# Kernel tuning notes

Hardware: AMD Instinct MI355X
Metric: run time of the kernel (lower is better)

Reference implementation:

```python
import jax, jax.numpy as jnp
import numpy as np

B, T, N, E = 8, 12, 10000, 160000
TD, OD = 64, 64  # temporal_dim, output_dim
EPS = 1e-5


def _ln(x, g, b):
    m = jnp.mean(x, axis=-1, keepdims=True)
    v = jnp.var(x, axis=-1, keepdims=True)
    return (x - m) * jax.lax.rsqrt(v + EPS) * g + b


def _gcn_agg(feat, src, dst, n_nodes):
    # feat: [B, N, D]; mean aggregation of src features into dst nodes
    msgs = feat[:, src, :]                                   # [B, E, D]
    deg = jnp.zeros((n_nodes,), feat.dtype).at[dst].add(1.0)  # [N]
    agg = jnp.zeros_like(feat).at[:, dst, :].add(msgs)        # [B, N, D]
    return agg / jnp.maximum(deg, 1.0)[None, :, None]


def setup_inputs() -> dict:
    key = jax.random.key(0)
    ks = jax.random.split(key, 20)
    s = 0.05
    rn = lambda k, shape: jax.random.normal(k, shape, jnp.float32) * s
    return {
        "x": jax.random.normal(ks[0], (B, T, N), jnp.float32),
        "edge_index": jax.random.randint(ks[1], (2, E), 0, N),
        "causal_edge_index": jax.random.randint(ks[2], (2, E), 0, N),
        # temporal branches (Linear over T)
        "W_ht": rn(ks[3], (T, TD)), "b_ht": jnp.zeros((TD,), jnp.float32),
        "W_lt": rn(ks[4], (T, TD)), "b_lt": jnp.zeros((TD,), jnp.float32),
        # high-freq spatial GCN
        "Ws_h": rn(ks[5], (TD, OD)), "Wn_h": rn(ks[6], (TD, OD)), "b_h": jnp.zeros((OD,), jnp.float32),
        # low-freq spatial GCN (base + causal graph)
        "Ws_l": rn(ks[7], (TD, OD)), "Wn_l": rn(ks[8], (TD, OD)), "Wc_l": rn(ks[9], (TD, OD)), "b_l": jnp.zeros((OD,), jnp.float32),
        # residual projections
        "Whr": rn(ks[10], (TD, OD)), "bhr": jnp.zeros((OD,), jnp.float32),
        "Wlr": rn(ks[11], (TD, OD)), "blr": jnp.zeros((OD,), jnp.float32),
        # layer norms
        "g_hn": jnp.ones((OD,), jnp.float32), "b_hn": jnp.zeros((OD,), jnp.float32),
        "g_ln": jnp.ones((OD,), jnp.float32), "b_ln": jnp.zeros((OD,), jnp.float32),
        # attention fusion gate
        "Wa": rn(ks[12], (2 * OD, 2)), "ba": jnp.zeros((2,), jnp.float32),
        # global residual
        "Wg": rn(ks[13], (T, OD)), "bg": jnp.zeros((OD,), jnp.float32),
        "g_gn": jnp.ones((OD,), jnp.float32), "b_gn": jnp.zeros((OD,), jnp.float32),
    }


def reference(x, edge_index, causal_edge_index,
              W_ht, b_ht, W_lt, b_lt,
              Ws_h, Wn_h, b_h, Ws_l, Wn_l, Wc_l, b_l,
              Whr, bhr, Wlr, blr,
              g_hn, b_hn, g_ln, b_ln,
              Wa, ba, Wg, bg, g_gn, b_gn):
    Bx, Tx, Nx = x.shape
    src, dst = edge_index[0], edge_index[1]
    csrc, cdst = causal_edge_index[0], causal_edge_index[1]
    x_for_residual = x + x  # low_src + high_src (both = x in source)

    # --- high-frequency branch ---
    ht = jnp.einsum('btn,td->bnd', x, W_ht) + b_ht          # [B, N, TD]
    agg_h = _gcn_agg(ht, src, dst, Nx)
    high = ht @ Ws_h + agg_h @ Wn_h + b_h                   # [B, N, OD]
    high = high + 0.2 * (ht @ Whr + bhr)
    high = _ln(high, g_hn, b_hn)
    high = jnp.where(high >= 0, high, 0.1 * high)           # leaky_relu(0.1)

    # --- low-frequency branch ---
    lt = jnp.einsum('btn,td->bnd', x, W_lt) + b_lt          # [B, N, TD]
    agg_l = _gcn_agg(lt, src, dst, Nx)
    agg_c = _gcn_agg(lt, csrc, cdst, Nx)
    low = lt @ Ws_l + agg_l @ Wn_l + agg_c @ Wc_l + b_l     # [B, N, OD]
    low = low + 0.2 * (lt @ Wlr + blr)
    low = _ln(low, g_ln, b_ln)
    low = jax.nn.gelu(low, approximate=False)

    # --- attention fusion ---
    logits = jnp.concatenate([high, low], axis=-1) @ Wa + ba  # [B, N, 2]
    a = jax.nn.softmax(logits, axis=-1)
    fused = a[..., 0:1] * high + a[..., 1:2] * low
    fused = fused + 0.3 * high + 0.3 * low

    # --- global residual ---
    residual = jnp.einsum('btn,td->bnd', x_for_residual, Wg) + bg
    residual = _ln(residual, g_gn, b_gn)
    fused = fused + 0.1 * residual

    # return in original [B, output_dim, N] layout
    return (jnp.swapaxes(fused, 1, 2), jnp.swapaxes(high, 1, 2), jnp.swapaxes(low, 1, 2))
```

## Files before the change

### kernel.cpp

```cpp
#include <hip/hip_runtime.h>

#define B_ 8
#define T_ 12
#define N_ 10000
#define E_ 160000
#define NQ_ 24
#define EPS_ 1e-5f
#define CAP_ 64
#define NC32 313
#define NT64 157

#define O_PAR     0
#define O_CURA    24576
#define O_CURC    65536
#define O_SLOTA   106496
#define O_SLOTC   2666496
#define O_XT      5226496

#define P_TAIL 4608

template<int CTRL>
__device__ __forceinline__ float dpp_add(float v) {
    int s = __builtin_amdgcn_update_dpp(0, __float_as_int(v), CTRL, 0xF, 0xF, true);
    return v + __int_as_float(s);
}
__device__ __forceinline__ float wave_sum(float v) {
    v = dpp_add<0x111>(v);
    v = dpp_add<0x112>(v);
    v = dpp_add<0x114>(v);
    v = dpp_add<0x118>(v);
    v = dpp_add<0x142>(v);
    v = dpp_add<0x143>(v);
    return __int_as_float(__builtin_amdgcn_readlane(__float_as_int(v), 63));
}

__device__ __forceinline__ void prep_task(int task,
    const float* W_ht, const float* W_lt,
    const float* Ws_h, const float* Wn_h,
    const float* Ws_l, const float* Wn_l, const float* Wc_l,
    const float* Whr, const float* Wlr,
    const float* Wg, float* par)
{
    int t = task >> 6, d = task & 63;
    float ah = 0.f, bh = 0.f, al = 0.f, bl = 0.f, cl = 0.f;
    for (int k = 0; k < 64; ++k) {
        float msh = Ws_h[k * 64 + d] + 0.2f * Whr[k * 64 + d];
        float msl = Ws_l[k * 64 + d] + 0.2f * Wlr[k * 64 + d];
        float wht = W_ht[t * 64 + k];
        float wlt = W_lt[t * 64 + k];
        ah += wht * msh;
        bh += wht * Wn_h[k * 64 + d];
        al += wlt * msl;
        bl += wlt * Wn_l[k * 64 + d];
        cl += wlt * Wc_l[k * 64 + d];
    }
    par[d * 72 + 0 * 12 + t] = ah;
    par[d * 72 + 1 * 12 + t] = bh;
    par[d * 72 + 2 * 12 + t] = al;
    par[d * 72 + 3 * 12 + t] = bl;
    par[d * 72 + 4 * 12 + t] = cl;
    par[d * 72 + 5 * 12 + t] = 2.f * Wg[t * 64 + d];
}

__device__ __forceinline__ void prep_tail(int d,
    const float* b_ht, const float* b_lt,
    const float* Ws_h, const float* Wn_h, const float* b_h,
    const float* Ws_l, const float* Wn_l, const float* Wc_l, const float* b_l,
    const float* Whr, const float* bhr, const float* Wlr, const float* blr,
    float* par)
{
    float ch0 = b_h[d] + 0.2f * bhr[d];
    float ch1 = 0.f;
    float cl0 = b_l[d] + 0.2f * blr[d];
    float cl1 = 0.f, cl2 = 0.f;
    for (int k = 0; k < 64; ++k) {
        float bht = b_ht[k];
        float blt = b_lt[k];
        float msh = Ws_h[k * 64 + d] + 0.2f * Whr[k * 64 + d];
        float msl = Ws_l[k * 64 + d] + 0.2f * Wlr[k * 64 + d];
        ch0 += bht * msh;
        ch1 += bht * Wn_h[k * 64 + d];
        cl0 += blt * msl;
        cl1 += blt * Wn_l[k * 64 + d];
        cl2 += blt * Wc_l[k * 64 + d];
    }
    par[P_TAIL + 0 * 64 + d] = ch0;
    par[P_TAIL + 1 * 64 + d] = ch1;
    par[P_TAIL + 2 * 64 + d] = cl0;
    par[P_TAIL + 3 * 64 + d] = cl1;
    par[P_TAIL + 4 * 64 + d] = cl2;
}

__global__ __launch_bounds__(256) void k1_kernel(
    const float* __restrict__ x, float* __restrict__ xt,
    const int* __restrict__ ei, const int* __restrict__ cei,
    int* __restrict__ curA, int* __restrict__ curC,
    int* __restrict__ slotA, int* __restrict__ slotC,
    const float* W_ht, const float* b_ht, const float* W_lt, const float* b_lt,
    const float* Ws_h, const float* Wn_h, const float* b_h,
    const float* Ws_l, const float* Wn_l, const float* Wc_l, const float* b_l,
    const float* Whr, const float* bhr, const float* Wlr, const float* blr,
    const float* Wg, float* par)
{
    __shared__ float tld[64 * 98];
    const int tid = threadIdx.x;
    const int blk = blockIdx.x;

    if (blk < NT64) {
        const int n0 = blk * 64;
        const int j = tid & 63;
        const int r0 = tid >> 6;
        const bool ok = (n0 + j) < N_;
#pragma unroll
        for (int rr = 0; rr < 24; ++rr) {
            int r = rr * 4 + r0;
            tld[j * 98 + r] = ok ? x[r * N_ + n0 + j] : 0.f;
        }
        __syncthreads();
        float4* xt4 = (float4*)xt;
#pragma unroll
        for (int it = 0; it < 6; ++it) {
            int idx = it * 256 + tid;
            int jj = idx / 24, q = idx - jj * 24;
            if (n0 + jj < N_) {
                float4 v;
                v.x = tld[jj * 98 + 4 * q + 0];
                v.y = tld[jj * 98 + 4 * q + 1];
                v.z = tld[jj * 98 + 4 * q + 2];
                v.w = tld[jj * 98 + 4 * q + 3];
                xt4[(size_t)(n0 + jj) * NQ_ + q] = v;
            }
        }
        return;
    }
    if (blk < NT64 + 3) {
        int task = (blk - NT64) * 256 + tid;
        prep_task(task, W_ht, W_lt, Ws_h, Wn_h, Ws_l, Wn_l, Wc_l, Whr, Wlr, Wg, par);
        return;
    }
    if (blk == NT64 + 3) {
        if (tid < 64)
            prep_tail(tid, b_ht, b_lt, Ws_h, Wn_h, b_h, Ws_l, Wn_l, Wc_l, b_l,
                      Whr, bhr, Wlr, blr, par);
        return;
    }
    int i = (blk - NT64 - 4) * 256 + tid;
    if (i < E_) {
        int dd = ei[E_ + i];
        int p = atomicAdd(&curA[dd], 1);
        if (p < CAP_) slotA[dd * CAP_ + p] = ei[i];
    } else if (i < 2 * E_) {
        int e = i - E_;
        int dd = cei[E_ + e];
        int p = atomicAdd(&curC[dd], 1);
        if (p < CAP_) slotC[dd * CAP_ + p] = cei[e];
    }
}

__global__ __launch_bounds__(256, 4) void main_kernel(
    const float* __restrict__ x, const float* __restrict__ par,
    const float4* __restrict__ xt4,
    const int* __restrict__ curA, const int* __restrict__ curC,
    const int* __restrict__ slotA, const int* __restrict__ slotC,
    const float* __restrict__ g_hn, const float* __restrict__ b_hn,
    const float* __restrict__ g_ln, const float* __restrict__ b_ln,
    const float* __restrict__ Wa, const float* __restrict__ ba,
    const float* __restrict__ bg, const float* __restrict__ g_gn,
    const float* __restrict__ b_gn,
    float* __restrict__ out)
{
    __shared__ __align__(16) float s_out[3][64 * 33];
    __shared__ __align__(16) float xs[32 * 12];
    __shared__ __align__(16) float as_[32 * 12];
    __shared__ __align__(16) float cs_[32 * 12];
    __shared__ float indA[32];
    __shared__ float indC[32];

    const int tid = threadIdx.x;
    const int lane = tid & 63;
    const int wave = tid >> 6;
    const int b = blockIdx.x & 7;
    const int n0 = (blockIdx.x >> 3) * 32;
    const int d = lane;

    {
        int idx = tid;
        int t = idx >> 5, node = idx & 31;
        int n = n0 + node;
        xs[node * 12 + t] = (n < N_) ? x[(b * T_ + t) * N_ + n] : 0.f;
        idx = tid + 256;
        if (idx < 384) {
            t = idx >> 5; node = idx & 31; n = n0 + node;
            xs[node * 12 + t] = (n < N_) ? x[(b * T_ + t) * N_ + n] : 0.f;
        }
    }

    {
        float4* P4 = (float4*)&s_out[0][0];
        const int p = tid >> 2;
        const int s = tid & 3;
        const int node = p & 31;
        const int set = p >> 5;
        const int n = n0 + node;
        float4 a0 = {0,0,0,0}, a1 = {0,0,0,0}, a2 = {0,0,0,0};
        if (n < N_) {
            const int* sl = (set ? slotC : slotA) + n * CAP_;
            int dgRaw = (set ? curC : curA)[n];
            int dg = dgRaw < CAP_ ? dgRaw : CAP_;
            for (int j = s; j < dg; j += 4) {
                const float4* src = xt4 + (size_t)sl[j] * NQ_ + b * 3;
                float4 v0 = src[0], v1 = src[1], v2 = src[2];
                a0.x += v0.x; a0.y += v0.y; a0.z += v0.z; a0.w += v0.w;
                a1.x += v1.x; a1.y += v1.y; a1.z += v1.z; a1.w += v1.w;
                a2.x += v2.x; a2.y += v2.y; a2.z += v2.z; a2.w += v2.w;
            }
        }
        P4[tid * 3 + 0] = a0;
        P4[tid * 3 + 1] = a1;
        P4[tid * 3 + 2] = a2;
    }
    __syncthreads();
    {
        const float4* P4 = (const float4*)&s_out[0][0];
        if (tid < 192) {
            int p2 = tid / 3, q = tid - p2 * 3;
            int node = p2 & 31, set = p2 >> 5;
            int n = n0 + node;
            float4 s0 = P4[(p2 * 4 + 0) * 3 + q];
            float4 s1 = P4[(p2 * 4 + 1) * 3 + q];
            float4 s2 = P4[(p2 * 4 + 2) * 3 + q];
            float4 s3 = P4[(p2 * 4 + 3) * 3 + q];
            float4 sum;
            sum.x = (s0.x + s1.x) + (s2.x + s3.x);
            sum.y = (s0.y + s1.y) + (s2.y + s3.y);
            sum.z = (s0.z + s1.z) + (s2.z + s3.z);
            sum.w = (s0.w + s1.w) + (s2.w + s3.w);
            int dgRaw = (n < N_) ? (set ? curC : curA)[n] : 0;
            float inv = 1.f / (float)(dgRaw > 0 ? dgRaw : 1);
            sum.x *= inv; sum.y *= inv; sum.z *= inv; sum.w *= inv;
            ((float4*)(set ? cs_ : as_))[node * 3 + q] = sum;
        } else {
            int i = tid - 192;
            int node = i & 31, set = i >> 5;
            int n = n0 + node;
            float f = (n < N_ && (set ? curC : curA)[n] > 0) ? 1.f : 0.f;
            if (set) indC[node] = f; else indA[node] = f;
        }
    }

    float w[72];
    {
        const float4* wv = (const float4*)(par + d * 72);
#pragma unroll
        for (int k = 0; k < 18; ++k) ((float4*)w)[k] = wv[k];
    }
    const float ch0 = par[P_TAIL + 0 * 64 + d], ch1 = par[P_TAIL + 1 * 64 + d];
    const float cl0 = par[P_TAIL + 2 * 64 + d], cl1 = par[P_TAIL + 3 * 64 + d];
    const float cl2 = par[P_TAIL + 4 * 64 + d];
    const float ghn = g_hn[d], bhn = b_hn[d];
    const float gln = g_ln[d], bln = b_ln[d];
    const float ggn = g_gn[d], bgn = b_gn[d];
    const float bgd = bg[d];
    const float wd0 = Wa[d * 2 + 0] - Wa[d * 2 + 1];
    const float wd1 = Wa[(64 + d) * 2 + 0] - Wa[(64 + d) * 2 + 1];
    const float bad = ba[0] - ba[1];

    __syncthreads();

#pragma unroll 2
    for (int i = 0; i < 8; ++i) {
        const int nl = wave * 8 + i;
        float u[12], ua[12], uc[12];
#pragma unroll
        for (int k = 0; k < 3; ++k) {
            ((float4*)u)[k]  = ((const float4*)(xs  + nl * 12))[k];
            ((float4*)ua)[k] = ((const float4*)(as_ + nl * 12))[k];
            ((float4*)uc)[k] = ((const float4*)(cs_ + nl * 12))[k];
        }
        const float indd = indA[nl], indc = indC[nl];

        float acc_h = ch0 + indd * ch1;
        float acc_l = cl0 + indd * cl1 + indc * cl2;
        float acc_r = bgd;
#pragma unroll
        for (int t = 0; t < 12; ++t) {
            acc_h += u[t] * w[t]      + ua[t] * w[12 + t];
            acc_l += u[t] * w[24 + t] + ua[t] * w[36 + t] + uc[t] * w[48 + t];
            acc_r += u[t] * w[60 + t];
        }

        float v0 = wave_sum(acc_h);
        float v1 = wave_sum(acc_h * acc_h);
        float v2 = wave_sum(acc_l);
        float v3 = wave_sum(acc_l * acc_l);
        float v4 = wave_sum(acc_r);
        float v5 = wave_sum(acc_r * acc_r);

        const float mh = v0 * (1.f / 64.f);
        const float varh = fmaxf(v1 * (1.f / 64.f) - mh * mh, 0.f);
        float hn = (acc_h - mh) * rsqrtf(varh + EPS_) * ghn + bhn;
        float high = hn >= 0.f ? hn : 0.1f * hn;

        const float ml = v2 * (1.f / 64.f);
        const float varl = fmaxf(v3 * (1.f / 64.f) - ml * ml, 0.f);
        float lnv = (acc_l - ml) * rsqrtf(varl + EPS_) * gln + bln;
        float low = 0.5f * lnv * (1.f + erff(lnv * 0.70710678118654752f));

        const float mr = v4 * (1.f / 64.f);
        const float varr = fmaxf(v5 * (1.f / 64.f) - mr * mr, 0.f);
        float rn = (acc_r - mr) * rsqrtf(varr + EPS_) * ggn + bgn;

        float S = wave_sum(high * wd0 + low * wd1);
        float a0 = 1.f / (1.f + expf(-(S + bad)));
        float fused = a0 * high + (1.f - a0) * low + 0.3f * high + 0.3f * low + 0.1f * rn;

        s_out[0][d * 33 + nl] = fused;
        s_out[1][d * 33 + nl] = high;
        s_out[2][d * 33 + nl] = low;
    }
    __syncthreads();

    const int off1 = B_ * 64 * N_;
    const int off2 = 2 * B_ * 64 * N_;
    for (int e2 = tid; e2 < 64 * 32; e2 += 256) {
        int r = e2 >> 5, nl = e2 & 31;
        int n = n0 + nl;
        if (n < N_) {
            float* o = out + (b * 64 + r) * N_ + n;
            o[0]    = s_out[0][r * 33 + nl];
            o[off1] = s_out[1][r * 33 + nl];
            o[off2] = s_out[2][r * 33 + nl];
        }
    }
}

extern "C" void kernel_launch(void* const* d_in, const int* in_sizes, int n_in,
                              void* d_out, int out_size, void* d_ws, size_t ws_size,
                              hipStream_t stream)
{
    const float* x   = (const float*)d_in[0];
    const int* ei    = (const int*)d_in[1];
    const int* cei   = (const int*)d_in[2];
    const float* W_ht = (const float*)d_in[3];
    const float* b_ht = (const float*)d_in[4];
    const float* W_lt = (const float*)d_in[5];
    const float* b_lt = (const float*)d_in[6];
    const float* Ws_h = (const float*)d_in[7];
    const float* Wn_h = (const float*)d_in[8];
    const float* b_h  = (const float*)d_in[9];
    const float* Ws_l = (const float*)d_in[10];
    const float* Wn_l = (const float*)d_in[11];
    const float* Wc_l = (const float*)d_in[12];
    const float* b_l  = (const float*)d_in[13];
    const float* Whr  = (const float*)d_in[14];
    const float* bhr  = (const float*)d_in[15];
    const float* Wlr  = (const float*)d_in[16];
    const float* blr  = (const float*)d_in[17];
    const float* g_hn = (const float*)d_in[18];
    const float* b_hn = (const float*)d_in[19];
    const float* g_ln = (const float*)d_in[20];
    const float* b_ln = (const float*)d_in[21];
    const float* Wa   = (const float*)d_in[22];
    const float* ba   = (const float*)d_in[23];
    const float* Wg   = (const float*)d_in[24];
    const float* bg   = (const float*)d_in[25];
    const float* g_gn = (const float*)d_in[26];
    const float* b_gn = (const float*)d_in[27];

    char* ws = (char*)d_ws;
    float* par   = (float*)(ws + O_PAR);
    int* curA    = (int*)(ws + O_CURA);
    int* curC    = (int*)(ws + O_CURC);
    int* slotA   = (int*)(ws + O_SLOTA);
    int* slotC   = (int*)(ws + O_SLOTC);
    float* xt    = (float*)(ws + O_XT);

    hipMemsetAsync(ws + O_CURA, 0, O_SLOTA - O_CURA, stream);

    k1_kernel<<<NT64 + 4 + (2 * E_ + 255) / 256, 256, 0, stream>>>(
        x, xt, ei, cei, curA, curC, slotA, slotC,
        W_ht, b_ht, W_lt, b_lt, Ws_h, Wn_h, b_h,
        Ws_l, Wn_l, Wc_l, b_l, Whr, bhr, Wlr, blr, Wg, par);

    main_kernel<<<NC32 * 8, 256, 0, stream>>>(
        x, par, (const float4*)xt, curA, curC, slotA, slotC,
        g_hn, b_hn, g_ln, b_ln, Wa, ba, bg, g_gn, b_gn, (float*)d_out);
}
```

Measured before the change: 208.5 us.

## Vectorize edge binning, unroll neighbor gather by two, use fast reciprocal/exp

Each thread in the edge-binning phase now loads four edges at once with int4 loads and issues four atomics, so the grid shrinks to match. The neighbor gather loop is unrolled to process two neighbors per iteration, which puts more loads in flight. The degree reciprocal and the attention sigmoid now use hardware rcp and fast exp intrinsics, and the high/low stores are moved ahead of the wave reduction. The fast intrinsics can slightly change numerics, and the int4 loads assume the edge arrays are 16-byte aligned.

```diff
diff --git a/kernel.cpp b/kernel.cpp
--- a/kernel.cpp
+++ b/kernel.cpp
@@ -144,16 +144,30 @@
                       Whr, bhr, Wlr, blr, par);
         return;
     }
-    int i = (blk - NT64 - 4) * 256 + tid;
-    if (i < E_) {
-        int dd = ei[E_ + i];
-        int p = atomicAdd(&curA[dd], 1);
-        if (p < CAP_) slotA[dd * CAP_ + p] = ei[i];
-    } else if (i < 2 * E_) {
-        int e = i - E_;
-        int dd = cei[E_ + e];
-        int p = atomicAdd(&curC[dd], 1);
-        if (p < CAP_) slotC[dd * CAP_ + p] = cei[e];
+    int e4 = (blk - NT64 - 4) * 256 + tid;
+    if (e4 < E_ / 4) {
+        int4 s4 = *(const int4*)&ei[4 * e4];
+        int4 d4 = *(const int4*)&ei[E_ + 4 * e4];
+        int p0 = atomicAdd(&curA[d4.x], 1);
+        int p1 = atomicAdd(&curA[d4.y], 1);
+        int p2 = atomicAdd(&curA[d4.z], 1);
+        int p3 = atomicAdd(&curA[d4.w], 1);
+        if (p0 < CAP_) slotA[d4.x * CAP_ + p0] = s4.x;
+        if (p1 < CAP_) slotA[d4.y * CAP_ + p1] = s4.y;
+        if (p2 < CAP_) slotA[d4.z * CAP_ + p2] = s4.z;
+        if (p3 < CAP_) slotA[d4.w * CAP_ + p3] = s4.w;
+    } else if (e4 < 2 * (E_ / 4)) {
+        int q = e4 - E_ / 4;
+        int4 s4 = *(const int4*)&cei[4 * q];
+        int4 d4 = *(const int4*)&cei[E_ + 4 * q];
+        int p0 = atomicAdd(&curC[d4.x], 1);
+        int p1 = atomicAdd(&curC[d4.y], 1);
+        int p2 = atomicAdd(&curC[d4.z], 1);
+        int p3 = atomicAdd(&curC[d4.w], 1);
+        if (p0 < CAP_) slotC[d4.x * CAP_ + p0] = s4.x;
+        if (p1 < CAP_) slotC[d4.y * CAP_ + p1] = s4.y;
+        if (p2 < CAP_) slotC[d4.z * CAP_ + p2] = s4.z;
+        if (p3 < CAP_) slotC[d4.w * CAP_ + p3] = s4.w;
     }
 }
 
@@ -207,7 +221,17 @@
             const int* sl = (set ? slotC : slotA) + n * CAP_;
             int dgRaw = (set ? curC : curA)[n];
             int dg = dgRaw < CAP_ ? dgRaw : CAP_;
-            for (int j = s; j < dg; j += 4) {
+            int j = s;
+            for (; j + 4 < dg; j += 8) {
+                const float4* src0 = xt4 + (size_t)sl[j]     * NQ_ + b * 3;
+                const float4* src1 = xt4 + (size_t)sl[j + 4] * NQ_ + b * 3;
+                float4 v0 = src0[0], v1 = src0[1], v2 = src0[2];
+                float4 v3 = src1[0], v4 = src1[1], v5 = src1[2];
+                a0.x += v0.x + v3.x; a0.y += v0.y + v3.y; a0.z += v0.z + v3.z; a0.w += v0.w + v3.w;
+                a1.x += v1.x + v4.x; a1.y += v1.y + v4.y; a1.z += v1.z + v4.z; a1.w += v1.w + v4.w;
+                a2.x += v2.x + v5.x; a2.y += v2.y + v5.y; a2.z += v2.z + v5.z; a2.w += v2.w + v5.w;
+            }
+            if (j < dg) {
                 const float4* src = xt4 + (size_t)sl[j] * NQ_ + b * 3;
                 float4 v0 = src[0], v1 = src[1], v2 = src[2];
                 a0.x += v0.x; a0.y += v0.y; a0.z += v0.z; a0.w += v0.w;
@@ -236,7 +260,7 @@
             sum.z = (s0.z + s1.z) + (s2.z + s3.z);
             sum.w = (s0.w + s1.w) + (s2.w + s3.w);
             int dgRaw = (n < N_) ? (set ? curC : curA)[n] : 0;
-            float inv = 1.f / (float)(dgRaw > 0 ? dgRaw : 1);
+            float inv = __builtin_amdgcn_rcpf((float)(dgRaw > 0 ? dgRaw : 1));
             sum.x *= inv; sum.y *= inv; sum.z *= inv; sum.w *= inv;
             ((float4*)(set ? cs_ : as_))[node * 3 + q] = sum;
         } else {
@@ -310,13 +334,14 @@
         const float varr = fmaxf(v5 * (1.f / 64.f) - mr * mr, 0.f);
         float rn = (acc_r - mr) * rsqrtf(varr + EPS_) * ggn + bgn;
 
-        float S = wave_sum(high * wd0 + low * wd1);
-        float a0 = 1.f / (1.f + expf(-(S + bad)));
-        float fused = a0 * high + (1.f - a0) * low + 0.3f * high + 0.3f * low + 0.1f * rn;
-
-        s_out[0][d * 33 + nl] = fused;
         s_out[1][d * 33 + nl] = high;
         s_out[2][d * 33 + nl] = low;
+
+        float S = wave_sum(high * wd0 + low * wd1);
+        float a0 = __builtin_amdgcn_rcpf(1.f + __expf(-(S + bad)));
+        float fused = a0 * high + (1.f - a0) * low + 0.3f * high + 0.3f * low + 0.1f * rn;
+
+        s_out[0][d * 33 + nl] = fused;
     }
     __syncthreads();
 
@@ -377,7 +402,7 @@
 
     hipMemsetAsync(ws + O_CURA, 0, O_SLOTA - O_CURA, stream);
 
-    k1_kernel<<<NT64 + 4 + (2 * E_ + 255) / 256, 256, 0, stream>>>(
+    k1_kernel<<<NT64 + 4 + 313, 256, 0, stream>>>(
         x, xt, ei, cei, curA, curC, slotA, slotC,
         W_ht, b_ht, W_lt, b_lt, Ws_h, Wn_h, b_h,
         Ws_l, Wn_l, Wc_l, b_l, Whr, bhr, Wlr, blr, Wg, par);
```

Measured after the change: 204.7 us. No clear change (-1.8%).
